# Kernel optimization log

Hardware: AMD Instinct MI355X
Metric: run time of the kernel (lower is better)

Reference implementation:

```python
import jax, jax.numpy as jnp
import numpy as np


def setup_inputs() -> dict:
    key = jax.random.key(0)
    ks = jax.random.split(key, 9)
    B, H = 8192, 1024
    scale = 1.0 / np.sqrt(4 * H)
    return {
        "h": jax.random.normal(ks[0], (B, H), jnp.float32),
        "x": jax.random.normal(ks[1], (B, 2 * H), jnp.float32),
        "glo": jax.random.normal(ks[2], (B, H), jnp.float32),
        "Wi_w": jax.random.normal(ks[3], (H, 4 * H), jnp.float32) * scale,
        "Wi_b": jnp.zeros((H,), jnp.float32),
        "Wf_w": jax.random.normal(ks[4], (H, 4 * H), jnp.float32) * scale,
        "Wf_b": jnp.zeros((H,), jnp.float32),
        "Wc_w": jax.random.normal(ks[5], (H, 4 * H), jnp.float32) * scale,
        "Wc_b": jnp.zeros((H,), jnp.float32),
    }


def reference(h, x, glo, Wi_w, Wi_b, Wf_w, Wf_b, Wc_w, Wc_b):
    # Dropout is identity in eval mode (deterministic reference).
    cat_all = jnp.concatenate([h, x, glo], axis=-1)  # [B, 4H]
    # Fused gate GEMM: stack the three weight matrices, one matmul.
    W = jnp.concatenate([Wi_w, Wf_w, Wc_w], axis=0)      # [3H, 4H]
    b = jnp.concatenate([Wi_b, Wf_b, Wc_b], axis=0)      # [3H]
    gates = cat_all @ W.T + b                             # [B, 3H]
    H = h.shape[-1]
    i = jax.nn.sigmoid(gates[:, :H])
    f = jax.nn.sigmoid(gates[:, H:2 * H])
    c = jnp.tanh(gates[:, 2 * H:])
    # 2-way softmax over (i, f): alpha0 = exp(i)/(exp(i)+exp(f)) = sigmoid(i-f)
    alpha0 = jax.nn.sigmoid(i - f)
    output = alpha0 * c + (1.0 - alpha0) * h
    return output
```

## Files before the change

kernel.cpp:

```cpp
#include <hip/hip_runtime.h>

typedef unsigned short USHORT;
typedef short bf16x8 __attribute__((ext_vector_type(8)));
typedef float f32x4 __attribute__((ext_vector_type(4)));

__device__ __forceinline__ USHORT f2bf(float f) {
    unsigned u = __float_as_uint(f);
    u += 0x7fffu + ((u >> 16) & 1u);
    return (USHORT)(u >> 16);
}
__device__ __forceinline__ float bf2f(USHORT s) {
    return __uint_as_float(((unsigned)s) << 16);
}
__device__ __forceinline__ float sigm(float v) { return 1.f / (1.f + __expf(-v)); }
__device__ __forceinline__ float mytanh(float v) { return 1.f - 2.f / (__expf(2.f * v) + 1.f); }

using gcu32p = const unsigned int __attribute__((address_space(1))) *;
using lu32p  = unsigned int __attribute__((address_space(3))) *;

__device__ __forceinline__ void load_lds16(const void* g, void* l) {
    __builtin_amdgcn_global_load_lds((gcu32p)g, (lu32p)l, 16, 0, 0);
}

__global__ __launch_bounds__(256) void conv_all(const float* __restrict__ h,
                                                const float* __restrict__ x,
                                                const float* __restrict__ glo,
                                                const float* __restrict__ Wi,
                                                const float* __restrict__ Wf,
                                                const float* __restrict__ Wc,
                                                USHORT* __restrict__ A,
                                                USHORT* __restrict__ W) {
    int bid = blockIdx.x;
    if (bid < 16384) {
        int idx = (bid * 256 + threadIdx.x) * 8;
        int m = idx >> 12, k = idx & 4095;
        const float* s;
        if (k < 1024)      s = h   + (size_t)m * 1024 + k;
        else if (k < 3072) s = x   + (size_t)m * 2048 + (k - 1024);
        else               s = glo + (size_t)m * 1024 + (k - 3072);
        float4 f0 = ((const float4*)s)[0];
        float4 f1 = ((const float4*)s)[1];
        union { USHORT us[8]; uint4 v; } u;
        u.us[0] = f2bf(f0.x); u.us[1] = f2bf(f0.y); u.us[2] = f2bf(f0.z); u.us[3] = f2bf(f0.w);
        u.us[4] = f2bf(f1.x); u.us[5] = f2bf(f1.y); u.us[6] = f2bf(f1.z); u.us[7] = f2bf(f1.w);
        *(uint4*)(A + idx) = u.v;
    } else {
        int idx = ((bid - 16384) * 256 + threadIdx.x) * 8;
        int n = idx >> 12, k = idx & 4095;
        const float* base = (n < 1024) ? Wi : (n < 2048 ? Wf : Wc);
        const float* s = base + (size_t)(n & 1023) * 4096 + k;
        float4 f0 = ((const float4*)s)[0];
        float4 f1 = ((const float4*)s)[1];
        union { USHORT us[8]; uint4 v; } u;
        u.us[0] = f2bf(f0.x); u.us[1] = f2bf(f0.y); u.us[2] = f2bf(f0.z); u.us[3] = f2bf(f0.w);
        u.us[4] = f2bf(f1.x); u.us[5] = f2bf(f1.y); u.us[6] = f2bf(f1.z); u.us[7] = f2bf(f1.w);
        *(uint4*)(W + idx) = u.v;
    }
}

__global__ __launch_bounds__(256) void gemm_bt(const USHORT* __restrict__ A,
                                               const USHORT* __restrict__ B,
                                               const float* __restrict__ bi,
                                               const float* __restrict__ bfp,
                                               const float* __restrict__ bc,
                                               USHORT* __restrict__ gates) {
    __shared__ USHORT At[128 * 64];
    __shared__ USHORT Bt[128 * 64];

    const int tid  = threadIdx.x;
    const int lane = tid & 63, wv = tid >> 6;
    const int bx = blockIdx.x;
    const int n0 = bx * 128;
    const int m0 = blockIdx.y * 128;
    const int wM = wv >> 1, wN = wv & 1;
    const int lm = lane & 15;
    const int gw = lane >> 4;
    const int swz0 = (((0 * 4 + gw) ^ (lm >> 1)) & 7) * 8;
    const int swz1 = (((1 * 4 + gw) ^ (lm >> 1)) & 7) * 8;

    const USHORT* aP[4];
    const USHORT* bP[4];
    USHORT* lA[4];
    USHORT* lB[4];
    #pragma unroll
    for (int j = 0; j < 4; ++j) {
        int c = wv + j * 4;
        int r = c * 8 + (lane >> 3);
        int g = (lane & 7) ^ ((r >> 1) & 7);
        lA[j] = At + c * 512;
        lB[j] = Bt + c * 512;
        aP[j] = A + (size_t)(m0 + r) * 4096 + g * 8;
        bP[j] = B + (size_t)(n0 + r) * 4096 + g * 8;
    }

    f32x4 acc[4][4];
    #pragma unroll
    for (int a = 0; a < 4; ++a)
        #pragma unroll
        for (int b = 0; b < 4; ++b) {
            f32x4 z = {0.f, 0.f, 0.f, 0.f};
            acc[a][b] = z;
        }

    for (int kt = 0; kt < 64; ++kt) {
        __syncthreads();
        #pragma unroll
        for (int j = 0; j < 4; ++j) load_lds16(aP[j], lA[j]);
        #pragma unroll
        for (int j = 0; j < 4; ++j) load_lds16(bP[j], lB[j]);
        #pragma unroll
        for (int j = 0; j < 4; ++j) { aP[j] += 64; bP[j] += 64; }
        __syncthreads();

        #pragma unroll
        for (int kh = 0; kh < 2; ++kh) {
            const int swz = kh ? swz1 : swz0;
            bf16x8 av[4], bv[4];
            #pragma unroll
            for (int mt = 0; mt < 4; ++mt)
                av[mt] = *(const bf16x8*)(At + (wM * 64 + mt * 16 + lm) * 64 + swz);
            #pragma unroll
            for (int nt = 0; nt < 4; ++nt)
                bv[nt] = *(const bf16x8*)(Bt + (wN * 64 + nt * 16 + lm) * 64 + swz);
            #pragma unroll
            for (int mt = 0; mt < 4; ++mt)
                #pragma unroll
                for (int nt = 0; nt < 4; ++nt)
                    acc[mt][nt] = __builtin_amdgcn_mfma_f32_16x16x32_bf16(
                        av[mt], bv[nt], acc[mt][nt], 0, 0, 0);
        }
    }

    const float* bias = (bx < 8) ? bi : (bx < 16 ? bfp : bc);
    const int boff = (bx & 7) * 128;
    #pragma unroll
    for (int nt = 0; nt < 4; ++nt) {
        int lcol = wN * 64 + nt * 16 + lm;
        float bb = bias[boff + lcol];
        #pragma unroll
        for (int mt = 0; mt < 4; ++mt) {
            #pragma unroll
            for (int r = 0; r < 4; ++r) {
                int lrow = wM * 64 + mt * 16 + (lane >> 4) * 4 + r;
                gates[(size_t)(m0 + lrow) * 3072 + n0 + lcol] = f2bf(acc[mt][nt][r] + bb);
            }
        }
    }
}

__global__ __launch_bounds__(256) void epi(const USHORT* __restrict__ gates,
                                           const float* __restrict__ h,
                                           float* __restrict__ out) {
    int e = (blockIdx.x * 256 + threadIdx.x) * 8;
    int m = e >> 10, n = e & 1023;
    const USHORT* gp = gates + (size_t)m * 3072 + n;
    union { USHORT us[8]; uint4 v; } gi, gf, gc;
    gi.v = *(const uint4*)(gp);
    gf.v = *(const uint4*)(gp + 1024);
    gc.v = *(const uint4*)(gp + 2048);
    const float* hp = h + (size_t)m * 1024 + n;
    float4 h0 = ((const float4*)hp)[0];
    float4 h1 = ((const float4*)hp)[1];
    float hv[8] = {h0.x, h0.y, h0.z, h0.w, h1.x, h1.y, h1.z, h1.w};
    float o[8];
    #pragma unroll
    for (int j = 0; j < 8; ++j) {
        float iv = sigm(bf2f(gi.us[j]));
        float fv = sigm(bf2f(gf.us[j]));
        float cv = mytanh(bf2f(gc.us[j]));
        float al = sigm(iv - fv);
        o[j] = al * cv + (1.f - al) * hv[j];
    }
    float4* op = (float4*)(out + (size_t)m * 1024 + n);
    op[0] = make_float4(o[0], o[1], o[2], o[3]);
    op[1] = make_float4(o[4], o[5], o[6], o[7]);
}

__global__ __launch_bounds__(256) void gemm3_noconv(const float* __restrict__ h,
                                                    const float* __restrict__ x,
                                                    const float* __restrict__ glo,
                                                    const float* __restrict__ Wi,
                                                    const float* __restrict__ Wf,
                                                    const float* __restrict__ Wc,
                                                    const float* __restrict__ bi,
                                                    const float* __restrict__ bfp,
                                                    const float* __restrict__ bc,
                                                    float* __restrict__ out) {
    __shared__ USHORT At[128 * 32];
    __shared__ USHORT Bt[128 * 32];
    __shared__ USHORT stash[128 * 136];

    const int tid  = threadIdx.x;
    const int lane = tid & 63, wv = tid >> 6;
    const int n0 = blockIdx.x * 128;
    const int m0 = blockIdx.y * 128;
    const int wM = wv >> 1, wN = wv & 1;
    const int lm = lane & 15, qk = (lane >> 4) * 8;
    const int rowS = tid >> 1;
    const int colS = (tid & 1) * 16;

    for (int p = 0; p < 3; ++p) {
        f32x4 acc[4][4];
        #pragma unroll
        for (int a = 0; a < 4; ++a)
            #pragma unroll
            for (int b = 0; b < 4; ++b) {
                f32x4 z = {0.f, 0.f, 0.f, 0.f};
                acc[a][b] = z;
            }
        const float* Wg = (p == 0) ? Wi : (p == 1 ? Wf : Wc);

        for (int kt = 0; kt < 128; ++kt) {
            __syncthreads();
            int k = kt * 32 + colS;
            const float* s;
            if (k < 1024)      s = h   + (size_t)(m0 + rowS) * 1024 + k;
            else if (k < 3072) s = x   + (size_t)(m0 + rowS) * 2048 + (k - 1024);
            else               s = glo + (size_t)(m0 + rowS) * 1024 + (k - 3072);
            float4 f0 = ((const float4*)s)[0], f1 = ((const float4*)s)[1];
            float4 f2 = ((const float4*)s)[2], f3 = ((const float4*)s)[3];
            union { USHORT us[8]; uint4 v; } u0, u1;
            u0.us[0]=f2bf(f0.x); u0.us[1]=f2bf(f0.y); u0.us[2]=f2bf(f0.z); u0.us[3]=f2bf(f0.w);
            u0.us[4]=f2bf(f1.x); u0.us[5]=f2bf(f1.y); u0.us[6]=f2bf(f1.z); u0.us[7]=f2bf(f1.w);
            u1.us[0]=f2bf(f2.x); u1.us[1]=f2bf(f2.y); u1.us[2]=f2bf(f2.z); u1.us[3]=f2bf(f2.w);
            u1.us[4]=f2bf(f3.x); u1.us[5]=f2bf(f3.y); u1.us[6]=f2bf(f3.z); u1.us[7]=f2bf(f3.w);
            *(uint4*)(At + rowS * 32 + colS)     = u0.v;
            *(uint4*)(At + rowS * 32 + colS + 8) = u1.v;
            const float* sw = Wg + (size_t)(n0 + rowS) * 4096 + k;
            float4 w0 = ((const float4*)sw)[0], w1 = ((const float4*)sw)[1];
            float4 w2 = ((const float4*)sw)[2], w3 = ((const float4*)sw)[3];
            union { USHORT us[8]; uint4 v; } v0, v1;
            v0.us[0]=f2bf(w0.x); v0.us[1]=f2bf(w0.y); v0.us[2]=f2bf(w0.z); v0.us[3]=f2bf(w0.w);
            v0.us[4]=f2bf(w1.x); v0.us[5]=f2bf(w1.y); v0.us[6]=f2bf(w1.z); v0.us[7]=f2bf(w1.w);
            v1.us[0]=f2bf(w2.x); v1.us[1]=f2bf(w2.y); v1.us[2]=f2bf(w2.z); v1.us[3]=f2bf(w2.w);
            v1.us[4]=f2bf(w3.x); v1.us[5]=f2bf(w3.y); v1.us[6]=f2bf(w3.z); v1.us[7]=f2bf(w3.w);
            *(uint4*)(Bt + rowS * 32 + colS)     = v0.v;
            *(uint4*)(Bt + rowS * 32 + colS + 8) = v1.v;
            __syncthreads();

            bf16x8 av[4], bv[4];
            #pragma unroll
            for (int mt = 0; mt < 4; ++mt)
                av[mt] = *(const bf16x8*)(At + (wM * 64 + mt * 16 + lm) * 32 + qk);
            #pragma unroll
            for (int nt = 0; nt < 4; ++nt)
                bv[nt] = *(const bf16x8*)(Bt + (wN * 64 + nt * 16 + lm) * 32 + qk);
            #pragma unroll
            for (int mt = 0; mt < 4; ++mt)
                #pragma unroll
                for (int nt = 0; nt < 4; ++nt)
                    acc[mt][nt] = __builtin_amdgcn_mfma_f32_16x16x32_bf16(
                        av[mt], bv[nt], acc[mt][nt], 0, 0, 0);
        }

        const float* bias = (p == 0) ? bi : (p == 1 ? bfp : bc);
        #pragma unroll
        for (int nt = 0; nt < 4; ++nt) {
            int lcol = wN * 64 + nt * 16 + lm;
            float bb = bias[n0 + lcol];
            #pragma unroll
            for (int mt = 0; mt < 4; ++mt) {
                #pragma unroll
                for (int r = 0; r < 4; ++r) {
                    int lrow = wM * 64 + mt * 16 + (lane >> 4) * 4 + r;
                    float g = acc[mt][nt][r] + bb;
                    int li = lrow * 136 + lcol;
                    if (p == 0) {
                        stash[li] = f2bf(sigm(g));
                    } else if (p == 1) {
                        float iv = bf2f(stash[li]);
                        stash[li] = f2bf(sigm(iv - sigm(g)));
                    } else {
                        float al = bf2f(stash[li]);
                        float cv = mytanh(g);
                        size_t gi = (size_t)(m0 + lrow) * 1024 + (n0 + lcol);
                        out[gi] = al * cv + (1.f - al) * h[gi];
                    }
                }
            }
        }
    }
}

extern "C" void kernel_launch(void* const* d_in, const int* in_sizes, int n_in,
                              void* d_out, int out_size, void* d_ws, size_t ws_size,
                              hipStream_t stream) {
    const float* h   = (const float*)d_in[0];
    const float* x   = (const float*)d_in[1];
    const float* glo = (const float*)d_in[2];
    const float* Wi  = (const float*)d_in[3];
    const float* bi  = (const float*)d_in[4];
    const float* Wf  = (const float*)d_in[5];
    const float* bfp = (const float*)d_in[6];
    const float* Wc  = (const float*)d_in[7];
    const float* bc  = (const float*)d_in[8];
    float* out = (float*)d_out;

    const size_t szA = (size_t)8192 * 4096 * 2;
    const size_t szW = (size_t)3072 * 4096 * 2;
    const size_t szG = (size_t)8192 * 3072 * 2;

    if (ws_size >= szA + szW + szG) {
        USHORT* Abf = (USHORT*)d_ws;
        USHORT* Wbf = (USHORT*)((char*)d_ws + szA);
        USHORT* Gbf = (USHORT*)((char*)d_ws + szA + szW);
        conv_all<<<16384 + 6144, 256, 0, stream>>>(h, x, glo, Wi, Wf, Wc, Abf, Wbf);
        gemm_bt<<<dim3(24, 64), 256, 0, stream>>>(Abf, Wbf, bi, bfp, bc, Gbf);
        epi<<<4096, 256, 0, stream>>>(Gbf, h, out);
    } else {
        gemm3_noconv<<<dim3(8, 64), 256, 0, stream>>>(
            h, x, glo, Wi, Wf, Wc, bi, bfp, bc, out);
    }
}
```

Baseline: 430.2 us.

## Replace GEMM with double-buffered 256x192 tile, 8-wave pipelined kernel

Replaces the 128x128 single-buffered bf16 GEMM with a 256x192 tile computed by 8 waves. The A and B tiles are double-buffered in LDS and the global-to-LDS loads are interleaved with the MFMA phases, using raw s_barrier, waitcnt and setprio for scheduling. It also remaps block IDs so neighbouring blocks share tiles, for better cache locality. The aim is to hide load latency behind compute and raise arithmetic intensity per block, at the cost of more registers and LDS (about 112KB) and fragile hand-tuned synchronisation.

```diff
diff --git a/kernel.cpp b/kernel.cpp
--- a/kernel.cpp
+++ b/kernel.cpp
@@ -58,91 +58,135 @@
     }
 }
 
-__global__ __launch_bounds__(256) void gemm_bt(const USHORT* __restrict__ A,
-                                               const USHORT* __restrict__ B,
-                                               const float* __restrict__ bi,
-                                               const float* __restrict__ bfp,
-                                               const float* __restrict__ bc,
-                                               USHORT* __restrict__ gates) {
-    __shared__ USHORT At[128 * 64];
-    __shared__ USHORT Bt[128 * 64];
+
+#define A_ELEMS 16384
+#define B_ELEMS 12288
+
+template<int AISS, int BISS, int WMODE>
+__device__ __forceinline__ void do_tile(int par, USHORT* As, USHORT* Bs,
+                                        const USHORT* (&aG)[4], const USHORT* (&bG)[3],
+                                        int wvOff, int aOff, int bOff, int koff0,
+                                        f32x4 (&acc)[8][3]) {
+    const USHORT* aRdp = As + par * A_ELEMS + aOff;
+    const USHORT* bRdp = Bs + par * B_ELEMS + bOff;
+    bf16x8 bv[3][2];
+    #pragma unroll
+    for (int q = 0; q < 4; ++q) {
+        bf16x8 av[2][2];
+        #pragma unroll
+        for (int m2 = 0; m2 < 2; ++m2)
+            #pragma unroll
+            for (int kh = 0; kh < 2; ++kh)
+                av[m2][kh] = *(const bf16x8*)(aRdp + (q * 32 + m2 * 16) * 64 + (koff0 ^ (kh * 32)));
+        if (q == 0) {
+            #pragma unroll
+            for (int nt = 0; nt < 3; ++nt)
+                #pragma unroll
+                for (int kh = 0; kh < 2; ++kh)
+                    bv[nt][kh] = *(const bf16x8*)(bRdp + nt * 16 * 64 + (koff0 ^ (kh * 32)));
+        }
+        if (AISS && q < 2) {
+            int j = q * 2;
+            load_lds16(aG[j],     As + (par ^ 1) * A_ELEMS + j * 4096 + wvOff);
+            load_lds16(aG[j + 1], As + (par ^ 1) * A_ELEMS + (j + 1) * 4096 + wvOff);
+            aG[j] += 64; aG[j + 1] += 64;
+        }
+        if (BISS && q == 2) {
+            load_lds16(bG[0], Bs + par * B_ELEMS + 0    + wvOff);
+            load_lds16(bG[1], Bs + par * B_ELEMS + 4096 + wvOff);
+            bG[0] += 64; bG[1] += 64;
+        }
+        if (BISS && q == 3) {
+            load_lds16(bG[2], Bs + par * B_ELEMS + 8192 + wvOff);
+            bG[2] += 64;
+        }
+        __builtin_amdgcn_sched_barrier(0);
+        __builtin_amdgcn_s_barrier();
+        __builtin_amdgcn_s_setprio(1);
+        #pragma unroll
+        for (int m2 = 0; m2 < 2; ++m2)
+            #pragma unroll
+            for (int nt = 0; nt < 3; ++nt)
+                #pragma unroll
+                for (int kh = 0; kh < 2; ++kh)
+                    acc[q * 2 + m2][nt] = __builtin_amdgcn_mfma_f32_16x16x32_bf16(
+                        av[m2][kh], bv[nt][kh], acc[q * 2 + m2][nt], 0, 0, 0);
+        __builtin_amdgcn_s_setprio(0);
+        if (q == 3) {
+            if (WMODE == 0) asm volatile("s_waitcnt vmcnt(3)" ::: "memory");
+            else if (WMODE == 1) asm volatile("s_waitcnt vmcnt(0)" ::: "memory");
+        }
+        __builtin_amdgcn_s_barrier();
+    }
+}
+
+__global__ __launch_bounds__(512, 2) void gemm8p(const USHORT* __restrict__ A,
+                                                 const USHORT* __restrict__ B,
+                                                 const float* __restrict__ bi,
+                                                 const float* __restrict__ bfp,
+                                                 const float* __restrict__ bc,
+                                                 USHORT* __restrict__ gates) {
+    __shared__ __align__(16) USHORT As[2 * 256 * 64];
+    __shared__ __align__(16) USHORT Bs[2 * 192 * 64];
 
     const int tid  = threadIdx.x;
     const int lane = tid & 63, wv = tid >> 6;
-    const int bx = blockIdx.x;
-    const int n0 = bx * 128;
-    const int m0 = blockIdx.y * 128;
-    const int wM = wv >> 1, wN = wv & 1;
+    const int s  = (blockIdx.x & 7) * 64 + (blockIdx.x >> 3);
+    const int m0 = (s & 31) * 256;
+    const int n0 = (s >> 5) * 192;
+
+    const int wM = wv >> 2, wN = wv & 3;
     const int lm = lane & 15;
     const int gw = lane >> 4;
-    const int swz0 = (((0 * 4 + gw) ^ (lm >> 1)) & 7) * 8;
-    const int swz1 = (((1 * 4 + gw) ^ (lm >> 1)) & 7) * 8;
-
-    const USHORT* aP[4];
-    const USHORT* bP[4];
-    USHORT* lA[4];
-    USHORT* lB[4];
-    #pragma unroll
-    for (int j = 0; j < 4; ++j) {
-        int c = wv + j * 4;
-        int r = c * 8 + (lane >> 3);
-        int g = (lane & 7) ^ ((r >> 1) & 7);
-        lA[j] = At + c * 512;
-        lB[j] = Bt + c * 512;
-        aP[j] = A + (size_t)(m0 + r) * 4096 + g * 8;
-        bP[j] = B + (size_t)(n0 + r) * 4096 + g * 8;
-    }
-
-    f32x4 acc[4][4];
-    #pragma unroll
-    for (int a = 0; a < 4; ++a)
-        #pragma unroll
-        for (int b = 0; b < 4; ++b) {
+    const int koff0 = ((gw ^ (lm >> 1)) & 7) * 8;
+    const int wvOff = wv * 512;
+    const int aOff = (wM * 128 + lm) * 64;
+    const int bOff = (wN * 48 + lm) * 64;
+
+    const int gswz = ((lane & 7) ^ (4 * (wv & 1) + (lane >> 4))) & 7;
+    const USHORT* aG[4];
+    const USHORT* bG[3];
+    #pragma unroll
+    for (int j = 0; j < 4; ++j)
+        aG[j] = A + (size_t)(m0 + j * 64 + wv * 8 + (lane >> 3)) * 4096 + gswz * 8;
+    #pragma unroll
+    for (int t = 0; t < 3; ++t)
+        bG[t] = B + (size_t)(n0 + t * 64 + wv * 8 + (lane >> 3)) * 4096 + gswz * 8;
+
+    f32x4 acc[8][3];
+    #pragma unroll
+    for (int a = 0; a < 8; ++a)
+        #pragma unroll
+        for (int b = 0; b < 3; ++b) {
             f32x4 z = {0.f, 0.f, 0.f, 0.f};
             acc[a][b] = z;
         }
 
-    for (int kt = 0; kt < 64; ++kt) {
-        __syncthreads();
-        #pragma unroll
-        for (int j = 0; j < 4; ++j) load_lds16(aP[j], lA[j]);
-        #pragma unroll
-        for (int j = 0; j < 4; ++j) load_lds16(bP[j], lB[j]);
-        #pragma unroll
-        for (int j = 0; j < 4; ++j) { aP[j] += 64; bP[j] += 64; }
-        __syncthreads();
-
-        #pragma unroll
-        for (int kh = 0; kh < 2; ++kh) {
-            const int swz = kh ? swz1 : swz0;
-            bf16x8 av[4], bv[4];
-            #pragma unroll
-            for (int mt = 0; mt < 4; ++mt)
-                av[mt] = *(const bf16x8*)(At + (wM * 64 + mt * 16 + lm) * 64 + swz);
-            #pragma unroll
-            for (int nt = 0; nt < 4; ++nt)
-                bv[nt] = *(const bf16x8*)(Bt + (wN * 64 + nt * 16 + lm) * 64 + swz);
-            #pragma unroll
-            for (int mt = 0; mt < 4; ++mt)
-                #pragma unroll
-                for (int nt = 0; nt < 4; ++nt)
-                    acc[mt][nt] = __builtin_amdgcn_mfma_f32_16x16x32_bf16(
-                        av[mt], bv[nt], acc[mt][nt], 0, 0, 0);
-        }
-    }
-
-    const float* bias = (bx < 8) ? bi : (bx < 16 ? bfp : bc);
-    const int boff = (bx & 7) * 128;
-    #pragma unroll
-    for (int nt = 0; nt < 4; ++nt) {
-        int lcol = wN * 64 + nt * 16 + lm;
-        float bb = bias[boff + lcol];
-        #pragma unroll
-        for (int mt = 0; mt < 4; ++mt) {
+    #pragma unroll
+    for (int j = 0; j < 4; ++j) { load_lds16(aG[j], As + j * 4096 + wvOff); aG[j] += 64; }
+    #pragma unroll
+    for (int t = 0; t < 3; ++t) { load_lds16(bG[t], Bs + t * 4096 + wvOff); bG[t] += 64; }
+    #pragma unroll
+    for (int t = 0; t < 3; ++t) { load_lds16(bG[t], Bs + B_ELEMS + t * 4096 + wvOff); bG[t] += 64; }
+    asm volatile("s_waitcnt vmcnt(3)" ::: "memory");
+    __builtin_amdgcn_s_barrier();
+
+    #pragma unroll 2
+    for (int kt = 0; kt < 62; ++kt)
+        do_tile<1, 1, 0>(kt & 1, As, Bs, aG, bG, wvOff, aOff, bOff, koff0, acc);
+    do_tile<1, 0, 1>(0, As, Bs, aG, bG, wvOff, aOff, bOff, koff0, acc);
+    do_tile<0, 0, 2>(1, As, Bs, aG, bG, wvOff, aOff, bOff, koff0, acc);
+
+    #pragma unroll
+    for (int nt = 0; nt < 3; ++nt) {
+        int gc = n0 + wN * 48 + nt * 16 + lm;
+        float bb = (gc < 1024) ? bi[gc] : (gc < 2048 ? bfp[gc - 1024] : bc[gc - 2048]);
+        #pragma unroll
+        for (int mt = 0; mt < 8; ++mt) {
             #pragma unroll
             for (int r = 0; r < 4; ++r) {
-                int lrow = wM * 64 + mt * 16 + (lane >> 4) * 4 + r;
-                gates[(size_t)(m0 + lrow) * 3072 + n0 + lcol] = f2bf(acc[mt][nt][r] + bb);
+                int lrow = wM * 128 + mt * 16 + (lane >> 4) * 4 + r;
+                gates[(size_t)(m0 + lrow) * 3072 + gc] = f2bf(acc[mt][nt][r] + bb);
             }
         }
     }
@@ -305,7 +349,7 @@
         USHORT* Wbf = (USHORT*)((char*)d_ws + szA);
         USHORT* Gbf = (USHORT*)((char*)d_ws + szA + szW);
         conv_all<<<16384 + 6144, 256, 0, stream>>>(h, x, glo, Wi, Wf, Wc, Abf, Wbf);
-        gemm_bt<<<dim3(24, 64), 256, 0, stream>>>(Abf, Wbf, bi, bfp, bc, Gbf);
+        gemm8p<<<512, 512, 0, stream>>>(Abf, Wbf, bi, bfp, bc, Gbf);
         epi<<<4096, 256, 0, stream>>>(Gbf, h, out);
     } else {
         gemm3_noconv<<<dim3(8, 64), 256, 0, stream>>>(
```

Measured after the change: 461.2 us. +7.2%, slower.
